# Optimization experiments

Measured on AMD Instinct MI355X. Metric: run time of the kernel, lower is better.

## Reference

```python
import jax, jax.numpy as jnp
import numpy as np
import math

NH = 16  # n_head
HS = 64  # head_size = n_embd // n_head


def setup_inputs() -> dict:
    key = jax.random.key(0)
    ks = jax.random.split(key, 7)
    B, T, C, QL, KVL = 2, 2048, 1024, 128, 128
    s = lambda k, shape, fan_in: jax.random.normal(k, shape, jnp.float32) / np.sqrt(fan_in)
    return {
        "x": jax.random.normal(ks[0], (B, T, C), jnp.float32),
        "W_dq": s(ks[1], (QL, C), C),
        "W_uq": s(ks[2], (C, QL), QL),
        "W_dkv": s(ks[3], (KVL, C), C),
        "W_uk": s(ks[4], (C, KVL), KVL),
        "W_uv": s(ks[5], (C, KVL), KVL),
        "W_o": s(ks[6], (C, C), C),
    }


def reference(x, W_dq, W_uq, W_dkv, W_uk, W_uv, W_o):
    B, T, C = x.shape
    kvl = W_dkv.shape[0]
    # absorbed matrices (training branch)
    k_eff = (W_dq.T @ W_uq.T @ W_uk).reshape(NH, HS, kvl)            # (nh, hs, kvl)
    v_eff = (W_uv.T @ W_o.T).reshape(kvl, NH, HS).transpose(1, 0, 2)  # (nh, kvl, hs)
    # latent kv cache
    c_kv = x @ W_dkv.T                                                # (B, T, kvl)
    # query path
    q = (x @ W_dq.T @ W_uq.T).reshape(B, T, NH, HS).transpose(0, 2, 1, 3)  # (B, nh, T, hs)
    # scores: q @ k_eff @ c_kv^T
    ql = jnp.einsum('bhtd,hdl->bhtl', q, k_eff)                       # (B, nh, T, kvl)
    scores = jnp.einsum('bhtl,bsl->bhts', ql, c_kv) / math.sqrt(HS)   # (B, nh, T, T)
    # causal mask
    mask = jnp.tril(jnp.ones((T, T), dtype=bool))
    scores = jnp.where(mask[None, None], scores, -jnp.inf)
    attn = jax.nn.softmax(scores, axis=-1)
    # output: attn @ c_kv @ v_eff
    ctx = jnp.einsum('bhts,bsl->bhtl', attn, c_kv)                    # (B, nh, T, kvl)
    y = jnp.einsum('bhtl,hld->bhtd', ctx, v_eff)                      # (B, nh, T, hs)
    y = y.transpose(0, 2, 1, 3).reshape(B, T, C)
    return y, c_kv
```

## Files before the change

### kernel.cpp

```cpp
#include <hip/hip_runtime.h>
#include <hip/hip_bf16.h>

typedef __hip_bfloat16 bf16;
typedef __attribute__((ext_vector_type(8))) short short8;
typedef __attribute__((ext_vector_type(4))) float f32x4;

#define NHD 16
#define HSD 64
#define KVLD 128
#define QLD 128
#define CD 1024
#define BD 2
#define TD 2048

__device__ __forceinline__ short8 ld8(const bf16* p) { return *(const short8*)p; }
__device__ __forceinline__ void st8(bf16* p, short8 v) { *(short8*)p = v; }

__device__ __forceinline__ void st4(bf16* p, float4 a) {
    union { short4 s; bf16 h[4]; } u;
    u.h[0] = __float2bfloat16(a.x); u.h[1] = __float2bfloat16(a.y);
    u.h[2] = __float2bfloat16(a.z); u.h[3] = __float2bfloat16(a.w);
    *(short4*)p = u.s;
}
__device__ __forceinline__ void st4f(bf16* p, f32x4 a) {
    union { short4 s; bf16 h[4]; } u;
    u.h[0] = __float2bfloat16(a[0]); u.h[1] = __float2bfloat16(a[1]);
    u.h[2] = __float2bfloat16(a[2]); u.h[3] = __float2bfloat16(a[3]);
    *(short4*)p = u.s;
}

__global__ __launch_bounds__(256) void k_pre(const float* __restrict__ wuq,
                                             const float* __restrict__ wuk,
                                             const float* __restrict__ wdq,
                                             const float* __restrict__ wdkv,
                                             float* __restrict__ m1p,
                                             float* __restrict__ G,
                                             bf16* __restrict__ wqkv_bf) {
    const int b = blockIdx.x;
    const int tid = threadIdx.x;
    if (b < 128) {
        const int part = b >> 4, ig = b & 15;
        const int i = ig * 8 + (tid >> 5);
        const int j4 = (tid & 31) << 2;
        const float* wq = wuq + (size_t)part * 128 * QLD;
        const float* wk = wuk + (size_t)part * 128 * KVLD;
        float4 acc = make_float4(0.f, 0.f, 0.f, 0.f);
        for (int c0 = 0; c0 < 128; c0 += 8) {
            float a[8]; float4 kv[8];
#pragma unroll
            for (int u = 0; u < 8; ++u) {
                a[u] = wq[(c0 + u) * QLD + i];
                kv[u] = *(const float4*)(wk + (c0 + u) * KVLD + j4);
            }
#pragma unroll
            for (int u = 0; u < 8; ++u) {
                acc.x = fmaf(a[u], kv[u].x, acc.x);
                acc.y = fmaf(a[u], kv[u].y, acc.y);
                acc.z = fmaf(a[u], kv[u].z, acc.z);
                acc.w = fmaf(a[u], kv[u].w, acc.w);
            }
        }
        *(float4*)(m1p + (size_t)part * 16384 + (size_t)i * 128 + j4) = acc;
    } else if (b < 256) {
        const int b1 = b - 128;
        const int h = b1 >> 3, p8 = b1 & 7;
        const int p = p8 * 16 + (tid >> 4);
        const int i8 = (tid & 15) << 3;
        float acc[8];
#pragma unroll
        for (int t = 0; t < 8; ++t) acc[t] = 0.f;
        const float* wdqp = wdq + (size_t)p * CD + h * 64;
        const float* wuqh = wuq + (size_t)(h * 64) * QLD + i8;
        for (int d0 = 0; d0 < 64; d0 += 8) {
            float a[8]; float4 b0[8], b1v[8];
#pragma unroll
            for (int u = 0; u < 8; ++u) {
                a[u] = wdqp[d0 + u];
                b0[u] = *(const float4*)(wuqh + (d0 + u) * QLD);
                b1v[u] = *(const float4*)(wuqh + (d0 + u) * QLD + 4);
            }
#pragma unroll
            for (int u = 0; u < 8; ++u) {
                acc[0] = fmaf(a[u], b0[u].x, acc[0]);  acc[1] = fmaf(a[u], b0[u].y, acc[1]);
                acc[2] = fmaf(a[u], b0[u].z, acc[2]);  acc[3] = fmaf(a[u], b0[u].w, acc[3]);
                acc[4] = fmaf(a[u], b1v[u].x, acc[4]); acc[5] = fmaf(a[u], b1v[u].y, acc[5]);
                acc[6] = fmaf(a[u], b1v[u].z, acc[6]); acc[7] = fmaf(a[u], b1v[u].w, acc[7]);
            }
        }
        float* dst = G + (size_t)h * 16384 + (size_t)p * 128 + i8;
        *(float4*)dst = make_float4(acc[0], acc[1], acc[2], acc[3]);
        *(float4*)(dst + 4) = make_float4(acc[4], acc[5], acc[6], acc[7]);
    } else {
        const int r = (b - 256) * 4 + (tid >> 6);
        const int lane = tid & 63;
        const float* src = (r < 128) ? (wdq + (size_t)r * CD) : (wdkv + (size_t)(r - 128) * CD);
        float4 f[4];
#pragma unroll
        for (int k = 0; k < 4; ++k) f[k] = ((const float4*)src)[lane + k * 64];
#pragma unroll
        for (int k = 0; k < 4; ++k)
            st4(wqkv_bf + (size_t)r * CD + (lane + k * 64) * 4, f[k]);
    }
}

__global__ __launch_bounds__(256) void k_main(const float* __restrict__ x,
                                              const bf16* __restrict__ wqkv_bf,
                                              const float* __restrict__ m1p,
                                              const float* __restrict__ G,
                                              const float* __restrict__ wuv,
                                              const float* __restrict__ wo,
                                              bf16* __restrict__ q1_bf,
                                              float* __restrict__ ckv_out,
                                              bf16* __restrict__ ckv_bf,
                                              bf16* __restrict__ ckvT_bf,
                                              bf16* __restrict__ Et_bf,
                                              bf16* __restrict__ veffT_bf) {
    __shared__ __align__(16) char arena[49152];
    const int blk = blockIdx.x;
    const int tid = threadIdx.x;

    if (blk < 256) {
        const int m0 = blk * 16;
        const int w = tid >> 6, lane = tid & 63, m16 = lane & 15, g = lane >> 4;
        bf16* As = (bf16*)arena;
        bf16* Bs = (bf16*)(arena + 2304);

        const int arow = tid >> 4, akc = (tid & 15) << 2;
        const float* axp = x + (size_t)(m0 + arow) * CD + akc;
        int brow[8], bkc[8];
#pragma unroll
        for (int kk = 0; kk < 8; ++kk) {
            int v = tid + kk * 256;
            brow[kk] = v >> 3; bkc[kk] = (v & 7) << 3;
        }

        float4 pA = *(const float4*)(axp);
        short8 pB[8];
#pragma unroll
        for (int kk = 0; kk < 8; ++kk)
            pB[kk] = ld8(wqkv_bf + (size_t)brow[kk] * CD + bkc[kk]);

        f32x4 acc[4];
#pragma unroll
        for (int nb = 0; nb < 4; ++nb) acc[nb] = (f32x4){0.f, 0.f, 0.f, 0.f};

        for (int k0 = 0; k0 < CD; k0 += 64) {
            __syncthreads();
            st4(As + arow * 72 + akc, pA);
#pragma unroll
            for (int kk = 0; kk < 8; ++kk)
                st8(Bs + brow[kk] * 72 + bkc[kk], pB[kk]);
            __syncthreads();
            if (k0 + 64 < CD) {
                pA = *(const float4*)(axp + k0 + 64);
#pragma unroll
                for (int kk = 0; kk < 8; ++kk)
                    pB[kk] = ld8(wqkv_bf + (size_t)brow[kk] * CD + k0 + 64 + bkc[kk]);
            }
            short8 aF[2];
#pragma unroll
            for (int kf = 0; kf < 2; ++kf)
                aF[kf] = ld8(As + m16 * 72 + kf * 32 + g * 8);
#pragma unroll
            for (int nb = 0; nb < 4; ++nb)
#pragma unroll
                for (int kf = 0; kf < 2; ++kf) {
                    short8 bF = ld8(Bs + (w * 64 + nb * 16 + m16) * 72 + kf * 32 + g * 8);
                    acc[nb] = __builtin_amdgcn_mfma_f32_16x16x32_bf16(aF[kf], bF, acc[nb], 0, 0, 0);
                }
        }

        const int bb = m0 >> 11;
        const int tl0 = (m0 & 2047) + g * 4;
#pragma unroll
        for (int nb = 0; nb < 4; ++nb) {
            int col = w * 64 + nb * 16 + m16;
            if (col < 128) {
#pragma unroll
                for (int r = 0; r < 4; ++r)
                    q1_bf[(size_t)(m0 + g * 4 + r) * QLD + col] = __float2bfloat16(acc[nb][r]);
            } else {
                int l = col - 128;
                union { short4 s; bf16 h[4]; } pk;
#pragma unroll
                for (int r = 0; r < 4; ++r) {
                    int t = m0 + g * 4 + r;
                    float v = acc[nb][r];
                    ckv_out[(size_t)t * KVLD + l] = v;
                    bf16 hv = __float2bfloat16(v);
                    ckv_bf[(size_t)t * KVLD + l] = hv;
                    pk.h[r] = hv;
                }
                *(short4*)(ckvT_bf + ((size_t)bb * KVLD + l) * TD + tl0) = pk.s;
            }
        }
    } else if (blk < 512) {
        const int b2 = blk - 256;
        const int h = b2 >> 4, lb = b2 & 15;
        float* m1s = (float*)arena;
        for (int v = tid; v < 1024; v += 256) {
            int p = v >> 3, lq = v & 7;
            float t0[8];
#pragma unroll
            for (int part = 0; part < 8; ++part)
                t0[part] = m1p[(size_t)part * 16384 + (size_t)p * 128 + lb * 8 + lq];
            float s0 = 0.f;
#pragma unroll
            for (int part = 0; part < 8; ++part) s0 += t0[part];
            m1s[v] = s0;
        }
        __syncthreads();
        const int lq = tid >> 5, i4 = (tid & 31) << 2;
        const float* Gh = G + (size_t)h * 16384;
        float4 acc = make_float4(0.f, 0.f, 0.f, 0.f);
        for (int p0 = 0; p0 < 128; p0 += 8) {
            float4 g[8]; float a[8];
#pragma unroll
            for (int u = 0; u < 8; ++u) {
                g[u] = *(const float4*)(Gh + (p0 + u) * 128 + i4);
                a[u] = m1s[(p0 + u) * 8 + lq];
            }
#pragma unroll
            for (int u = 0; u < 8; ++u) {
                acc.x = fmaf(a[u], g[u].x, acc.x);
                acc.y = fmaf(a[u], g[u].y, acc.y);
                acc.z = fmaf(a[u], g[u].z, acc.z);
                acc.w = fmaf(a[u], g[u].w, acc.w);
            }
        }
        const float sc = 0.1803368801f;
        const int l = lb * 8 + lq;
        st4(Et_bf + ((size_t)h * 128 + l) * 128 + i4,
            make_float4(sc * acc.x, sc * acc.y, sc * acc.z, sc * acc.w));
    } else {
        const int b3 = blk - 512;
        const int cc0 = b3 * 4;
        float* woS = (float*)arena;
        float* wuvS = (float*)arena + 4096;
#pragma unroll
        for (int k = 0; k < 4; ++k)
            ((float4*)woS)[tid + k * 256] = ((const float4*)(wo + (size_t)cc0 * CD))[tid + k * 256];

        const int r = tid >> 6;
        const int lh = tid & 63;
        float4 pf[8];
#pragma unroll
        for (int t = 0; t < 8; ++t)
            pf[t] = ((const float4*)wuv)[t * 256 + tid];

        float a0 = 0.f, a1 = 0.f;
        for (int ch = 0; ch < 16; ++ch) {
            __syncthreads();
#pragma unroll
            for (int t = 0; t < 8; ++t)
                ((float4*)wuvS)[t * 256 + tid] = pf[t];
            __syncthreads();
            if (ch < 15) {
#pragma unroll
                for (int t = 0; t < 8; ++t)
                    pf[t] = ((const float4*)wuv)[(ch + 1) * 2048 + t * 256 + tid];
            }
            const float* wr = woS + r * 1024 + ch * 64;
            const float2* vv = (const float2*)wuvS + lh;
            for (int cb = 0; cb < 64; cb += 8) {
                float wv[8]; float2 v[8];
#pragma unroll
                for (int u = 0; u < 8; ++u) {
                    wv[u] = wr[cb + u];
                    v[u] = vv[(cb + u) * 64];
                }
#pragma unroll
                for (int u = 0; u < 8; ++u) {
                    a0 = fmaf(wv[u], v[u].x, a0);
                    a1 = fmaf(wv[u], v[u].y, a1);
                }
            }
        }
        union { short2 s; bf16 h2[2]; } u;
        u.h2[0] = __float2bfloat16(a0);
        u.h2[1] = __float2bfloat16(a1);
        *(short2*)(veffT_bf + (size_t)(cc0 + r) * KVLD + lh * 2) = u.s;
    }
}

__global__ __launch_bounds__(512, 4) void k_flash(const bf16* __restrict__ Q1_bf,
                                                  const bf16* __restrict__ Et_bf,
                                                  const bf16* __restrict__ ckv_bf,
                                                  const bf16* __restrict__ ckvT_bf,
                                                  const bf16* __restrict__ veffT_bf,
                                                  float* __restrict__ yout) {
    const int h = blockIdx.x & 15;
    const int b = blockIdx.x >> 4;
    const int qlo = blockIdx.y;
    const int qhi = 31 - qlo;
    const int tid = threadIdx.x;
    const int w = tid >> 6;
    const int ws = w >> 2;
    const int wq = w & 3;
    const int lane = tid & 63;
    const int m16 = lane & 15;
    const int g = lane >> 4;
    const int myqt = ws ? qlo : qhi;
    const int row0 = myqt * 64;

    __shared__ __align__(16) short smem_raw[28288];
    bf16* smem = (bf16*)smem_raw;
    bf16* kvN = smem;
    bf16* kvT = smem + 8704;
    bf16* pS  = smem + 19072 + w * 1152;
    bf16* bufLo = kvT;
    bf16* vT = smem + 19072;

    {
        const bf16 one = __float2bfloat16(1.0f);
        for (int idx = tid; idx < 16 * 72; idx += 512)
            kvT[9216 + idx] = one;
    }

    {
        const bf16* q1hi = Q1_bf + ((size_t)(b * TD + qhi * 64)) * QLD;
        const bf16* q1lo = Q1_bf + ((size_t)(b * TD + qlo * 64)) * QLD;
#pragma unroll
        for (int k = 0; k < 2; ++k) {
            int v = tid + k * 512;
            int row = v >> 4, cv = (v & 15) << 3;
            st8(kvN + row * 136 + cv, ld8(q1hi + row * QLD + cv));
            st8(bufLo + row * 136 + cv, ld8(q1lo + row * QLD + cv));
        }
    }
    __syncthreads();
    bf16* myQ1 = ws ? bufLo : kvN;
    {
        short8 aq[4];
#pragma unroll
        for (int kf = 0; kf < 4; ++kf)
            aq[kf] = ld8(myQ1 + (wq * 16 + m16) * 136 + kf * 32 + g * 8);
        const bf16* Eh = Et_bf + (size_t)h * QLD * KVLD;
        f32x4 qc[8];
#pragma unroll
        for (int nb = 0; nb < 8; ++nb) qc[nb] = (f32x4){0.f, 0.f, 0.f, 0.f};
#pragma unroll
        for (int nb = 0; nb < 8; ++nb)
#pragma unroll
            for (int kf = 0; kf < 4; ++kf) {
                short8 bq = ld8(Eh + (nb * 16 + m16) * QLD + kf * 32 + g * 8);
                qc[nb] = __builtin_amdgcn_mfma_f32_16x16x32_bf16(bq, aq[kf], qc[nb], 0, 0, 0);
            }
        __syncthreads();
#pragma unroll
        for (int nb = 0; nb < 8; ++nb)
            st4f(myQ1 + (wq * 16 + m16) * 136 + nb * 16 + g * 4, qc[nb]);
    }
    __syncthreads();
    short8 qlA[4];
#pragma unroll
    for (int kf = 0; kf < 4; ++kf)
        qlA[kf] = ld8(myQ1 + (wq * 16 + m16) * 136 + kf * 32 + g * 8);

    f32x4 cx[9];
#pragma unroll
    for (int nb = 0; nb < 9; ++nb) cx[nb] = (f32x4){0.f, 0.f, 0.f, 0.f};
    float mrow = -INFINITY;
    const int rg = row0 + wq * 16 + m16;

    const bf16* ckb = ckv_bf + (size_t)b * TD * KVLD;
    const bf16* ckTb = ckvT_bf + (size_t)b * KVLD * TD;

    int nrow[2], ncol[2], trow[2], tcol[2];
#pragma unroll
    for (int k = 0; k < 2; ++k) {
        int v = tid + k * 512;
        nrow[k] = v >> 4; ncol[k] = (v & 15) << 3;
        trow[k] = v >> 3; tcol[k] = (v & 7) << 3;
    }
    short8 pfN[2], pfT[2];
#pragma unroll
    for (int k = 0; k < 2; ++k) {
        pfN[k] = ld8(ckb + (size_t)nrow[k] * KVLD + ncol[k]);
        pfT[k] = ld8(ckTb + (size_t)trow[k] * TD + tcol[k]);
    }

    for (int tile = 0; tile <= qhi; ++tile) {
        const int s0 = tile * 64;
        __syncthreads();
#pragma unroll
        for (int k = 0; k < 2; ++k) {
            st8(kvN + nrow[k] * 136 + ncol[k], pfN[k]);
            st8(kvT + trow[k] * 72 + tcol[k], pfT[k]);
        }
        __syncthreads();
        if (tile < qhi) {
            const int s1 = s0 + 64;
#pragma unroll
            for (int k = 0; k < 2; ++k) {
                pfN[k] = ld8(ckb + (size_t)(s1 + nrow[k]) * KVLD + ncol[k]);
                pfT[k] = ld8(ckTb + (size_t)trow[k] * TD + s1 + tcol[k]);
            }
        }

        if (ws == 0 || tile <= qlo) {
            f32x4 sa[4];
#pragma unroll
            for (int nb = 0; nb < 4; ++nb) sa[nb] = (f32x4){0.f, 0.f, 0.f, 0.f};
#pragma unroll
            for (int nb = 0; nb < 4; ++nb)
#pragma unroll
                for (int kf = 0; kf < 4; ++kf) {
                    short8 ak = ld8(kvN + (nb * 16 + m16) * 136 + kf * 32 + g * 8);
                    sa[nb] = __builtin_amdgcn_mfma_f32_16x16x32_bf16(ak, qlA[kf], sa[nb], 0, 0, 0);
                }

            if (tile == myqt) {
#pragma unroll
                for (int nb = 0; nb < 4; ++nb)
#pragma unroll
                    for (int r = 0; r < 4; ++r) {
                        int sg = s0 + nb * 16 + g * 4 + r;
                        if (sg > rg) sa[nb][r] = -INFINITY;
                    }
            }

            float mloc = sa[0][0];
#pragma unroll
            for (int nb = 0; nb < 4; ++nb)
#pragma unroll
                for (int r = 0; r < 4; ++r) mloc = fmaxf(mloc, sa[nb][r]);
            mloc = fmaxf(mloc, __shfl_xor(mloc, 16));
            mloc = fmaxf(mloc, __shfl_xor(mloc, 32));
            if (__any(mloc > mrow + 8.f)) {
                float mt = fmaxf(mrow, mloc);
                float al = exp2f(mrow - mt);
                mrow = mt;
#pragma unroll
                for (int nb = 0; nb < 9; ++nb)
#pragma unroll
                    for (int r = 0; r < 4; ++r) cx[nb][r] *= al;
            }

#pragma unroll
            for (int nb = 0; nb < 4; ++nb) {
                float4 p4;
                p4.x = exp2f(sa[nb][0] - mrow);
                p4.y = exp2f(sa[nb][1] - mrow);
                p4.z = exp2f(sa[nb][2] - mrow);
                p4.w = exp2f(sa[nb][3] - mrow);
                st4(pS + m16 * 72 + nb * 16 + g * 4, p4);
            }
            __builtin_amdgcn_wave_barrier();

            short8 pA[2];
#pragma unroll
            for (int kf = 0; kf < 2; ++kf)
                pA[kf] = ld8(pS + m16 * 72 + kf * 32 + g * 8);
#pragma unroll
            for (int nb = 0; nb < 9; ++nb)
#pragma unroll
                for (int kf = 0; kf < 2; ++kf) {
                    short8 av = ld8(kvT + (nb * 16 + m16) * 72 + kf * 32 + g * 8);
                    cx[nb] = __builtin_amdgcn_mfma_f32_16x16x32_bf16(av, pA[kf], cx[nb], 0, 0, 0);
                }
        }
    }

    float invl = 1.f / cx[8][0];
#pragma unroll
    for (int nb = 0; nb < 8; ++nb)
#pragma unroll
        for (int r = 0; r < 4; ++r) cx[nb][r] *= invl;
    __syncthreads();
    bf16* ctxS = ws ? bufLo : kvN;
#pragma unroll
    for (int nb = 0; nb < 8; ++nb)
        st4f(ctxS + (wq * 16 + m16) * 136 + nb * 16 + g * 4, cx[nb]);
    {
        const bf16* vsrc = veffT_bf + (size_t)h * HSD * KVLD;
#pragma unroll
        for (int k = 0; k < 2; ++k) {
            int v = tid + k * 512;
            int row = v >> 4, cv = (v & 15) << 3;
            st8(vT + row * 136 + cv, ld8(vsrc + row * KVLD + cv));
        }
    }
    __syncthreads();

    short8 cB[4];
#pragma unroll
    for (int kf = 0; kf < 4; ++kf)
        cB[kf] = ld8(ctxS + (wq * 16 + m16) * 136 + kf * 32 + g * 8);
    f32x4 ya[4];
#pragma unroll
    for (int nb = 0; nb < 4; ++nb) ya[nb] = (f32x4){0.f, 0.f, 0.f, 0.f};
#pragma unroll
    for (int nb = 0; nb < 4; ++nb)
#pragma unroll
        for (int kf = 0; kf < 4; ++kf) {
            short8 av = ld8(vT + (nb * 16 + m16) * 136 + kf * 32 + g * 8);
            ya[nb] = __builtin_amdgcn_mfma_f32_16x16x32_bf16(av, cB[kf], ya[nb], 0, 0, 0);
        }
    float* yo = yout + ((size_t)b * TD + rg) * CD + h * HSD;
#pragma unroll
    for (int nb = 0; nb < 4; ++nb)
        *(float4*)(yo + nb * 16 + g * 4) = *(float4*)&ya[nb];
}

extern "C" void kernel_launch(void* const* d_in, const int* in_sizes, int n_in,
                              void* d_out, int out_size, void* d_ws, size_t ws_size,
                              hipStream_t stream) {
    const float* x    = (const float*)d_in[0];
    const float* wdq  = (const float*)d_in[1];
    const float* wuq  = (const float*)d_in[2];
    const float* wdkv = (const float*)d_in[3];
    const float* wuk  = (const float*)d_in[4];
    const float* wuv  = (const float*)d_in[5];
    const float* wo   = (const float*)d_in[6];
    float* yout = (float*)d_out;
    float* ckv_out = yout + (size_t)BD * TD * CD;

    float* ws = (float*)d_ws;
    float* M1P = ws;
    float* G   = M1P + 131072;
    bf16* wqkv_bf  = (bf16*)(G + 262144);
    bf16* Et_bf    = wqkv_bf + 262144;
    bf16* veffT_bf = Et_bf + 262144;
    bf16* ckv_bf   = veffT_bf + 131072;
    bf16* ckvT_bf  = ckv_bf + 524288;
    bf16* Q1_bf    = ckvT_bf + 524288;

    k_pre <<<320, 256, 0, stream>>>(wuq, wuk, wdq, wdkv, M1P, G, wqkv_bf);
    k_main<<<768, 256, 0, stream>>>(x, wqkv_bf, M1P, G, wuv, wo,
                                    Q1_bf, ckv_out, ckv_bf, ckvT_bf, Et_bf, veffT_bf);

    dim3 grid(32, 16);
    k_flash<<<grid, 512, 0, stream>>>(Q1_bf, Et_bf, ckv_bf, ckvT_bf, veffT_bf, yout);
}
```

Before: 221.1 us.

## Compute softmax denominator in registers, move v_eff prep to k_pre, add MFMA priority

The flash kernel no longer gets the row sum from a ninth MFMA block against a ones row in shared memory. It now accumulates the denominator from the exponentials with two cross-lane shuffles, which removes one of nine PV MFMA groups per tile and shrinks shared memory. The v_eff transpose product moves from k_main into k_pre, so k_main uses less LDS and launches fewer blocks, while k_pre grows and its blocks need 48KB LDS. s_setprio wraps the MFMA loops to favour matrix issue across waves.

```diff
diff --git a/kernel.cpp b/kernel.cpp
--- a/kernel.cpp
+++ b/kernel.cpp
@@ -33,9 +33,13 @@
                                              const float* __restrict__ wuk,
                                              const float* __restrict__ wdq,
                                              const float* __restrict__ wdkv,
+                                             const float* __restrict__ wuv,
+                                             const float* __restrict__ wo,
                                              float* __restrict__ m1p,
                                              float* __restrict__ G,
-                                             bf16* __restrict__ wqkv_bf) {
+                                             bf16* __restrict__ wqkv_bf,
+                                             bf16* __restrict__ veffT_bf) {
+    __shared__ __align__(16) char arena[49152];
     const int b = blockIdx.x;
     const int tid = threadIdx.x;
     if (b < 128) {
@@ -90,7 +94,7 @@
         float* dst = G + (size_t)h * 16384 + (size_t)p * 128 + i8;
         *(float4*)dst = make_float4(acc[0], acc[1], acc[2], acc[3]);
         *(float4*)(dst + 4) = make_float4(acc[4], acc[5], acc[6], acc[7]);
-    } else {
+    } else if (b < 320) {
         const int r = (b - 256) * 4 + (tid >> 6);
         const int lane = tid & 63;
         const float* src = (r < 128) ? (wdq + (size_t)r * CD) : (wdkv + (size_t)(r - 128) * CD);
@@ -100,6 +104,54 @@
 #pragma unroll
         for (int k = 0; k < 4; ++k)
             st4(wqkv_bf + (size_t)r * CD + (lane + k * 64) * 4, f[k]);
+    } else {
+        const int b3 = b - 320;
+        const int cc0 = b3 * 4;
+        float* woS = (float*)arena;
+        float* wuvS = (float*)arena + 4096;
+#pragma unroll
+        for (int k = 0; k < 4; ++k)
+            ((float4*)woS)[tid + k * 256] = ((const float4*)(wo + (size_t)cc0 * CD))[tid + k * 256];
+
+        const int r = tid >> 6;
+        const int lh = tid & 63;
+        float4 pf[8];
+#pragma unroll
+        for (int t = 0; t < 8; ++t)
+            pf[t] = ((const float4*)wuv)[t * 256 + tid];
+
+        float a0 = 0.f, a1 = 0.f;
+        for (int ch = 0; ch < 16; ++ch) {
+            __syncthreads();
+#pragma unroll
+            for (int t = 0; t < 8; ++t)
+                ((float4*)wuvS)[t * 256 + tid] = pf[t];
+            __syncthreads();
+            if (ch < 15) {
+#pragma unroll
+                for (int t = 0; t < 8; ++t)
+                    pf[t] = ((const float4*)wuv)[(ch + 1) * 2048 + t * 256 + tid];
+            }
+            const float* wr = woS + r * 1024 + ch * 64;
+            const float2* vv = (const float2*)wuvS + lh;
+            for (int cb = 0; cb < 64; cb += 8) {
+                float wv[8]; float2 v[8];
+#pragma unroll
+                for (int u = 0; u < 8; ++u) {
+                    wv[u] = wr[cb + u];
+                    v[u] = vv[(cb + u) * 64];
+                }
+#pragma unroll
+                for (int u = 0; u < 8; ++u) {
+                    a0 = fmaf(wv[u], v[u].x, a0);
+                    a1 = fmaf(wv[u], v[u].y, a1);
+                }
+            }
+        }
+        union { short2 s; bf16 h2[2]; } u;
+        u.h2[0] = __float2bfloat16(a0);
+        u.h2[1] = __float2bfloat16(a1);
+        *(short2*)(veffT_bf + (size_t)(cc0 + r) * KVLD + lh * 2) = u.s;
     }
 }
 
@@ -107,15 +159,12 @@
                                               const bf16* __restrict__ wqkv_bf,
                                               const float* __restrict__ m1p,
                                               const float* __restrict__ G,
-                                              const float* __restrict__ wuv,
-                                              const float* __restrict__ wo,
                                               bf16* __restrict__ q1_bf,
                                               float* __restrict__ ckv_out,
                                               bf16* __restrict__ ckv_bf,
                                               bf16* __restrict__ ckvT_bf,
-                                              bf16* __restrict__ Et_bf,
-                                              bf16* __restrict__ veffT_bf) {
-    __shared__ __align__(16) char arena[49152];
+                                              bf16* __restrict__ Et_bf) {
+    __shared__ __align__(16) char arena[39168];
     const int blk = blockIdx.x;
     const int tid = threadIdx.x;
 
@@ -194,7 +243,7 @@
                 *(short4*)(ckvT_bf + ((size_t)bb * KVLD + l) * TD + tl0) = pk.s;
             }
         }
-    } else if (blk < 512) {
+    } else {
         const int b2 = blk - 256;
         const int h = b2 >> 4, lb = b2 & 15;
         float* m1s = (float*)arena;
@@ -232,54 +281,6 @@
         const int l = lb * 8 + lq;
         st4(Et_bf + ((size_t)h * 128 + l) * 128 + i4,
             make_float4(sc * acc.x, sc * acc.y, sc * acc.z, sc * acc.w));
-    } else {
-        const int b3 = blk - 512;
-        const int cc0 = b3 * 4;
-        float* woS = (float*)arena;
-        float* wuvS = (float*)arena + 4096;
-#pragma unroll
-        for (int k = 0; k < 4; ++k)
-            ((float4*)woS)[tid + k * 256] = ((const float4*)(wo + (size_t)cc0 * CD))[tid + k * 256];
-
-        const int r = tid >> 6;
-        const int lh = tid & 63;
-        float4 pf[8];
-#pragma unroll
-        for (int t = 0; t < 8; ++t)
-            pf[t] = ((const float4*)wuv)[t * 256 + tid];
-
-        float a0 = 0.f, a1 = 0.f;
-        for (int ch = 0; ch < 16; ++ch) {
-            __syncthreads();
-#pragma unroll
-            for (int t = 0; t < 8; ++t)
-                ((float4*)wuvS)[t * 256 + tid] = pf[t];
-            __syncthreads();
-            if (ch < 15) {
-#pragma unroll
-                for (int t = 0; t < 8; ++t)
-                    pf[t] = ((const float4*)wuv)[(ch + 1) * 2048 + t * 256 + tid];
-            }
-            const float* wr = woS + r * 1024 + ch * 64;
-            const float2* vv = (const float2*)wuvS + lh;
-            for (int cb = 0; cb < 64; cb += 8) {
-                float wv[8]; float2 v[8];
-#pragma unroll
-                for (int u = 0; u < 8; ++u) {
-                    wv[u] = wr[cb + u];
-                    v[u] = vv[(cb + u) * 64];
-                }
-#pragma unroll
-                for (int u = 0; u < 8; ++u) {
-                    a0 = fmaf(wv[u], v[u].x, a0);
-                    a1 = fmaf(wv[u], v[u].y, a1);
-                }
-            }
-        }
-        union { short2 s; bf16 h2[2]; } u;
-        u.h2[0] = __float2bfloat16(a0);
-        u.h2[1] = __float2bfloat16(a1);
-        *(short2*)(veffT_bf + (size_t)(cc0 + r) * KVLD + lh * 2) = u.s;
     }
 }
 
@@ -303,19 +304,13 @@
     const int myqt = ws ? qlo : qhi;
     const int row0 = myqt * 64;
 
-    __shared__ __align__(16) short smem_raw[28288];
+    __shared__ __align__(16) short smem_raw[27136];
     bf16* smem = (bf16*)smem_raw;
     bf16* kvN = smem;
     bf16* kvT = smem + 8704;
-    bf16* pS  = smem + 19072 + w * 1152;
+    bf16* pS  = smem + 17920 + w * 1152;
     bf16* bufLo = kvT;
-    bf16* vT = smem + 19072;
-
-    {
-        const bf16 one = __float2bfloat16(1.0f);
-        for (int idx = tid; idx < 16 * 72; idx += 512)
-            kvT[9216 + idx] = one;
-    }
+    bf16* vT = smem + 17920;
 
     {
         const bf16* q1hi = Q1_bf + ((size_t)(b * TD + qhi * 64)) * QLD;
@@ -357,9 +352,10 @@
     for (int kf = 0; kf < 4; ++kf)
         qlA[kf] = ld8(myQ1 + (wq * 16 + m16) * 136 + kf * 32 + g * 8);
 
-    f32x4 cx[9];
-#pragma unroll
-    for (int nb = 0; nb < 9; ++nb) cx[nb] = (f32x4){0.f, 0.f, 0.f, 0.f};
+    f32x4 cx[8];
+#pragma unroll
+    for (int nb = 0; nb < 8; ++nb) cx[nb] = (f32x4){0.f, 0.f, 0.f, 0.f};
+    float den = 0.f;
     float mrow = -INFINITY;
     const int rg = row0 + wq * 16 + m16;
 
@@ -402,6 +398,7 @@
             f32x4 sa[4];
 #pragma unroll
             for (int nb = 0; nb < 4; ++nb) sa[nb] = (f32x4){0.f, 0.f, 0.f, 0.f};
+            __builtin_amdgcn_s_setprio(1);
 #pragma unroll
             for (int nb = 0; nb < 4; ++nb)
 #pragma unroll
@@ -409,6 +406,7 @@
                     short8 ak = ld8(kvN + (nb * 16 + m16) * 136 + kf * 32 + g * 8);
                     sa[nb] = __builtin_amdgcn_mfma_f32_16x16x32_bf16(ak, qlA[kf], sa[nb], 0, 0, 0);
                 }
+            __builtin_amdgcn_s_setprio(0);
 
             if (tile == myqt) {
 #pragma unroll
@@ -431,12 +429,14 @@
                 float mt = fmaxf(mrow, mloc);
                 float al = exp2f(mrow - mt);
                 mrow = mt;
-#pragma unroll
-                for (int nb = 0; nb < 9; ++nb)
+                den *= al;
+#pragma unroll
+                for (int nb = 0; nb < 8; ++nb)
 #pragma unroll
                     for (int r = 0; r < 4; ++r) cx[nb][r] *= al;
             }
 
+            float psum = 0.f;
 #pragma unroll
             for (int nb = 0; nb < 4; ++nb) {
                 float4 p4;
@@ -444,25 +444,31 @@
                 p4.y = exp2f(sa[nb][1] - mrow);
                 p4.z = exp2f(sa[nb][2] - mrow);
                 p4.w = exp2f(sa[nb][3] - mrow);
+                psum += (p4.x + p4.y) + (p4.z + p4.w);
                 st4(pS + m16 * 72 + nb * 16 + g * 4, p4);
             }
+            psum += __shfl_xor(psum, 16);
+            psum += __shfl_xor(psum, 32);
+            den += psum;
             __builtin_amdgcn_wave_barrier();
 
             short8 pA[2];
 #pragma unroll
             for (int kf = 0; kf < 2; ++kf)
                 pA[kf] = ld8(pS + m16 * 72 + kf * 32 + g * 8);
-#pragma unroll
-            for (int nb = 0; nb < 9; ++nb)
+            __builtin_amdgcn_s_setprio(1);
+#pragma unroll
+            for (int nb = 0; nb < 8; ++nb)
 #pragma unroll
                 for (int kf = 0; kf < 2; ++kf) {
                     short8 av = ld8(kvT + (nb * 16 + m16) * 72 + kf * 32 + g * 8);
                     cx[nb] = __builtin_amdgcn_mfma_f32_16x16x32_bf16(av, pA[kf], cx[nb], 0, 0, 0);
                 }
-        }
-    }
-
-    float invl = 1.f / cx[8][0];
+            __builtin_amdgcn_s_setprio(0);
+        }
+    }
+
+    float invl = 1.f / den;
 #pragma unroll
     for (int nb = 0; nb < 8; ++nb)
 #pragma unroll
@@ -526,9 +532,10 @@
     bf16* ckvT_bf  = ckv_bf + 524288;
     bf16* Q1_bf    = ckvT_bf + 524288;
 
-    k_pre <<<320, 256, 0, stream>>>(wuq, wuk, wdq, wdkv, M1P, G, wqkv_bf);
-    k_main<<<768, 256, 0, stream>>>(x, wqkv_bf, M1P, G, wuv, wo,
-                                    Q1_bf, ckv_out, ckv_bf, ckvT_bf, Et_bf, veffT_bf);
+    k_pre <<<576, 256, 0, stream>>>(wuq, wuk, wdq, wdkv, wuv, wo,
+                                    M1P, G, wqkv_bf, veffT_bf);
+    k_main<<<512, 256, 0, stream>>>(x, wqkv_bf, M1P, G,
+                                    Q1_bf, ckv_out, ckv_bf, ckvT_bf, Et_bf);
 
     dim3 grid(32, 16);
     k_flash<<<grid, 512, 0, stream>>>(Q1_bf, Et_bf, ckv_bf, ckvT_bf, veffT_bf, yout);
```

Result: no change. 224.7 us (+1.6%).

## Split paired causal tiles into per-tile blocks and shuffle P through registers

Applied to the files above, without the earlier changes.

Each flash block now handles a single 64-row query tile with 256 threads, instead of pairing a high and a low tile in a 512-thread block. The grid doubles and is ordered heaviest-first. The softmax denominator is now summed explicitly in registers, replacing the extra all-ones column MFMA (9 to 8 output blocks). P is moved between lanes with cross-lane shuffles into MFMA operand layout instead of going through a per-wave LDS scratch buffer. This removes LDS round-trips and an MFMA per tile and cuts shared memory per block, at the cost of losing the balanced pairing and adding many shuffle instructions.

```diff
diff --git a/kernel.cpp b/kernel.cpp
--- a/kernel.cpp
+++ b/kernel.cpp
@@ -27,6 +27,11 @@
     u.h[0] = __float2bfloat16(a[0]); u.h[1] = __float2bfloat16(a[1]);
     u.h[2] = __float2bfloat16(a[2]); u.h[3] = __float2bfloat16(a[3]);
     *(short4*)p = u.s;
+}
+__device__ __forceinline__ unsigned pk2(float x, float y) {
+    union { unsigned u; bf16 h[2]; } t;
+    t.h[0] = __float2bfloat16(x); t.h[1] = __float2bfloat16(y);
+    return t.u;
 }
 
 __global__ __launch_bounds__(256) void k_pre(const float* __restrict__ wuq,
@@ -283,7 +288,7 @@
     }
 }
 
-__global__ __launch_bounds__(512, 4) void k_flash(const bf16* __restrict__ Q1_bf,
+__global__ __launch_bounds__(256, 4) void k_flash(const bf16* __restrict__ Q1_bf,
                                                   const bf16* __restrict__ Et_bf,
                                                   const bf16* __restrict__ ckv_bf,
                                                   const bf16* __restrict__ ckvT_bf,
@@ -291,50 +296,35 @@
                                                   float* __restrict__ yout) {
     const int h = blockIdx.x & 15;
     const int b = blockIdx.x >> 4;
-    const int qlo = blockIdx.y;
-    const int qhi = 31 - qlo;
+    const int qt = 31 - blockIdx.y;
     const int tid = threadIdx.x;
-    const int w = tid >> 6;
-    const int ws = w >> 2;
-    const int wq = w & 3;
+    const int wq = tid >> 6;
     const int lane = tid & 63;
     const int m16 = lane & 15;
     const int g = lane >> 4;
-    const int myqt = ws ? qlo : qhi;
-    const int row0 = myqt * 64;
-
-    __shared__ __align__(16) short smem_raw[28288];
+    const int row0 = qt * 64;
+
+    __shared__ __align__(16) short smem_raw[17920];
     bf16* smem = (bf16*)smem_raw;
     bf16* kvN = smem;
     bf16* kvT = smem + 8704;
-    bf16* pS  = smem + 19072 + w * 1152;
-    bf16* bufLo = kvT;
-    bf16* vT = smem + 19072;
+    bf16* vT  = kvT;
 
     {
-        const bf16 one = __float2bfloat16(1.0f);
-        for (int idx = tid; idx < 16 * 72; idx += 512)
-            kvT[9216 + idx] = one;
-    }
-
-    {
-        const bf16* q1hi = Q1_bf + ((size_t)(b * TD + qhi * 64)) * QLD;
-        const bf16* q1lo = Q1_bf + ((size_t)(b * TD + qlo * 64)) * QLD;
-#pragma unroll
-        for (int k = 0; k < 2; ++k) {
-            int v = tid + k * 512;
+        const bf16* q1p = Q1_bf + ((size_t)(b * TD + row0)) * QLD;
+#pragma unroll
+        for (int k = 0; k < 4; ++k) {
+            int v = tid + k * 256;
             int row = v >> 4, cv = (v & 15) << 3;
-            st8(kvN + row * 136 + cv, ld8(q1hi + row * QLD + cv));
-            st8(bufLo + row * 136 + cv, ld8(q1lo + row * QLD + cv));
+            st8(kvN + row * 136 + cv, ld8(q1p + row * QLD + cv));
         }
     }
     __syncthreads();
-    bf16* myQ1 = ws ? bufLo : kvN;
     {
         short8 aq[4];
 #pragma unroll
         for (int kf = 0; kf < 4; ++kf)
-            aq[kf] = ld8(myQ1 + (wq * 16 + m16) * 136 + kf * 32 + g * 8);
+            aq[kf] = ld8(kvN + (wq * 16 + m16) * 136 + kf * 32 + g * 8);
         const bf16* Eh = Et_bf + (size_t)h * QLD * KVLD;
         f32x4 qc[8];
 #pragma unroll
@@ -349,134 +339,157 @@
         __syncthreads();
 #pragma unroll
         for (int nb = 0; nb < 8; ++nb)
-            st4f(myQ1 + (wq * 16 + m16) * 136 + nb * 16 + g * 4, qc[nb]);
+            st4f(kvN + (wq * 16 + m16) * 136 + nb * 16 + g * 4, qc[nb]);
     }
     __syncthreads();
     short8 qlA[4];
 #pragma unroll
     for (int kf = 0; kf < 4; ++kf)
-        qlA[kf] = ld8(myQ1 + (wq * 16 + m16) * 136 + kf * 32 + g * 8);
-
-    f32x4 cx[9];
-#pragma unroll
-    for (int nb = 0; nb < 9; ++nb) cx[nb] = (f32x4){0.f, 0.f, 0.f, 0.f};
+        qlA[kf] = ld8(kvN + (wq * 16 + m16) * 136 + kf * 32 + g * 8);
+
+    f32x4 cx[8];
+#pragma unroll
+    for (int nb = 0; nb < 8; ++nb) cx[nb] = (f32x4){0.f, 0.f, 0.f, 0.f};
+    float den = 0.f;
     float mrow = -INFINITY;
     const int rg = row0 + wq * 16 + m16;
 
     const bf16* ckb = ckv_bf + (size_t)b * TD * KVLD;
     const bf16* ckTb = ckvT_bf + (size_t)b * KVLD * TD;
 
-    int nrow[2], ncol[2], trow[2], tcol[2];
-#pragma unroll
-    for (int k = 0; k < 2; ++k) {
-        int v = tid + k * 512;
+    int nrow[4], ncol[4], trow[4], tcol[4];
+#pragma unroll
+    for (int k = 0; k < 4; ++k) {
+        int v = tid + k * 256;
         nrow[k] = v >> 4; ncol[k] = (v & 15) << 3;
         trow[k] = v >> 3; tcol[k] = (v & 7) << 3;
     }
-    short8 pfN[2], pfT[2];
-#pragma unroll
-    for (int k = 0; k < 2; ++k) {
+    short8 pfN[4], pfT[4];
+#pragma unroll
+    for (int k = 0; k < 4; ++k) {
         pfN[k] = ld8(ckb + (size_t)nrow[k] * KVLD + ncol[k]);
         pfT[k] = ld8(ckTb + (size_t)trow[k] * TD + tcol[k]);
     }
 
-    for (int tile = 0; tile <= qhi; ++tile) {
-        const int s0 = tile * 64;
+    const int sA = (((2 * g) & 3) << 4) + m16;
+    const int sB = (((2 * g + 1) & 3) << 4) + m16;
+    const int hi = g >> 1;
+
+    for (int tile = 0; tile <= qt; ++tile) {
         __syncthreads();
 #pragma unroll
-        for (int k = 0; k < 2; ++k) {
+        for (int k = 0; k < 4; ++k) {
             st8(kvN + nrow[k] * 136 + ncol[k], pfN[k]);
             st8(kvT + trow[k] * 72 + tcol[k], pfT[k]);
         }
         __syncthreads();
-        if (tile < qhi) {
-            const int s1 = s0 + 64;
-#pragma unroll
-            for (int k = 0; k < 2; ++k) {
+        if (tile < qt) {
+            const int s1 = (tile + 1) * 64;
+#pragma unroll
+            for (int k = 0; k < 4; ++k) {
                 pfN[k] = ld8(ckb + (size_t)(s1 + nrow[k]) * KVLD + ncol[k]);
                 pfT[k] = ld8(ckTb + (size_t)trow[k] * TD + s1 + tcol[k]);
             }
         }
 
-        if (ws == 0 || tile <= qlo) {
-            f32x4 sa[4];
-#pragma unroll
-            for (int nb = 0; nb < 4; ++nb) sa[nb] = (f32x4){0.f, 0.f, 0.f, 0.f};
+        f32x4 sa[4];
+#pragma unroll
+        for (int nb = 0; nb < 4; ++nb) sa[nb] = (f32x4){0.f, 0.f, 0.f, 0.f};
+#pragma unroll
+        for (int nb = 0; nb < 4; ++nb)
+#pragma unroll
+            for (int kf = 0; kf < 4; ++kf) {
+                short8 ak = ld8(kvN + (nb * 16 + m16) * 136 + kf * 32 + g * 8);
+                sa[nb] = __builtin_amdgcn_mfma_f32_16x16x32_bf16(ak, qlA[kf], sa[nb], 0, 0, 0);
+            }
+
+        if (tile == qt) {
+            const int s0 = tile * 64;
 #pragma unroll
             for (int nb = 0; nb < 4; ++nb)
 #pragma unroll
-                for (int kf = 0; kf < 4; ++kf) {
-                    short8 ak = ld8(kvN + (nb * 16 + m16) * 136 + kf * 32 + g * 8);
-                    sa[nb] = __builtin_amdgcn_mfma_f32_16x16x32_bf16(ak, qlA[kf], sa[nb], 0, 0, 0);
+                for (int r = 0; r < 4; ++r) {
+                    int sg = s0 + nb * 16 + g * 4 + r;
+                    if (sg > rg) sa[nb][r] = -INFINITY;
                 }
-
-            if (tile == myqt) {
-#pragma unroll
-                for (int nb = 0; nb < 4; ++nb)
-#pragma unroll
-                    for (int r = 0; r < 4; ++r) {
-                        int sg = s0 + nb * 16 + g * 4 + r;
-                        if (sg > rg) sa[nb][r] = -INFINITY;
-                    }
-            }
-
-            float mloc = sa[0][0];
-#pragma unroll
-            for (int nb = 0; nb < 4; ++nb)
-#pragma unroll
-                for (int r = 0; r < 4; ++r) mloc = fmaxf(mloc, sa[nb][r]);
-            mloc = fmaxf(mloc, __shfl_xor(mloc, 16));
-            mloc = fmaxf(mloc, __shfl_xor(mloc, 32));
-            if (__any(mloc > mrow + 8.f)) {
-                float mt = fmaxf(mrow, mloc);
-                float al = exp2f(mrow - mt);
-                mrow = mt;
-#pragma unroll
-                for (int nb = 0; nb < 9; ++nb)
-#pragma unroll
-                    for (int r = 0; r < 4; ++r) cx[nb][r] *= al;
-            }
-
-#pragma unroll
-            for (int nb = 0; nb < 4; ++nb) {
-                float4 p4;
-                p4.x = exp2f(sa[nb][0] - mrow);
-                p4.y = exp2f(sa[nb][1] - mrow);
-                p4.z = exp2f(sa[nb][2] - mrow);
-                p4.w = exp2f(sa[nb][3] - mrow);
-                st4(pS + m16 * 72 + nb * 16 + g * 4, p4);
-            }
-            __builtin_amdgcn_wave_barrier();
-
-            short8 pA[2];
-#pragma unroll
-            for (int kf = 0; kf < 2; ++kf)
-                pA[kf] = ld8(pS + m16 * 72 + kf * 32 + g * 8);
-#pragma unroll
-            for (int nb = 0; nb < 9; ++nb)
-#pragma unroll
-                for (int kf = 0; kf < 2; ++kf) {
-                    short8 av = ld8(kvT + (nb * 16 + m16) * 72 + kf * 32 + g * 8);
-                    cx[nb] = __builtin_amdgcn_mfma_f32_16x16x32_bf16(av, pA[kf], cx[nb], 0, 0, 0);
-                }
-        }
-    }
-
-    float invl = 1.f / cx[8][0];
+        }
+
+        float mloc = sa[0][0];
+#pragma unroll
+        for (int nb = 0; nb < 4; ++nb)
+#pragma unroll
+            for (int r = 0; r < 4; ++r) mloc = fmaxf(mloc, sa[nb][r]);
+        mloc = fmaxf(mloc, __shfl_xor(mloc, 16));
+        mloc = fmaxf(mloc, __shfl_xor(mloc, 32));
+        if (__any(mloc > mrow + 8.f)) {
+            float mt = fmaxf(mrow, mloc);
+            float al = exp2f(mrow - mt);
+            mrow = mt;
+            den *= al;
+#pragma unroll
+            for (int nb = 0; nb < 8; ++nb)
+#pragma unroll
+                for (int r = 0; r < 4; ++r) cx[nb][r] *= al;
+        }
+
+        unsigned w_[4][2];
+        float psum = 0.f;
+#pragma unroll
+        for (int nb = 0; nb < 4; ++nb) {
+            float p0 = exp2f(sa[nb][0] - mrow);
+            float p1 = exp2f(sa[nb][1] - mrow);
+            float p2 = exp2f(sa[nb][2] - mrow);
+            float p3 = exp2f(sa[nb][3] - mrow);
+            psum += (p0 + p1) + (p2 + p3);
+            w_[nb][0] = pk2(p0, p1);
+            w_[nb][1] = pk2(p2, p3);
+        }
+        psum += __shfl_xor(psum, 16);
+        psum += __shfl_xor(psum, 32);
+        den += psum;
+
+        short8 pA[2];
+#pragma unroll
+        for (int kf = 0; kf < 2; ++kf) {
+            unsigned a0 = (unsigned)__shfl((int)w_[2 * kf][0], sA);
+            unsigned b0 = (unsigned)__shfl((int)w_[2 * kf + 1][0], sA);
+            unsigned a1 = (unsigned)__shfl((int)w_[2 * kf][1], sA);
+            unsigned b1 = (unsigned)__shfl((int)w_[2 * kf + 1][1], sA);
+            unsigned a2 = (unsigned)__shfl((int)w_[2 * kf][0], sB);
+            unsigned b2 = (unsigned)__shfl((int)w_[2 * kf + 1][0], sB);
+            unsigned a3 = (unsigned)__shfl((int)w_[2 * kf][1], sB);
+            unsigned b3 = (unsigned)__shfl((int)w_[2 * kf + 1][1], sB);
+            union { short8 s8; unsigned u[4]; } pb;
+            pb.u[0] = hi ? b0 : a0;
+            pb.u[1] = hi ? b1 : a1;
+            pb.u[2] = hi ? b2 : a2;
+            pb.u[3] = hi ? b3 : a3;
+            pA[kf] = pb.s8;
+        }
+
+#pragma unroll
+        for (int nb = 0; nb < 8; ++nb)
+#pragma unroll
+            for (int kf = 0; kf < 2; ++kf) {
+                short8 av = ld8(kvT + (nb * 16 + m16) * 72 + kf * 32 + g * 8);
+                cx[nb] = __builtin_amdgcn_mfma_f32_16x16x32_bf16(av, pA[kf], cx[nb], 0, 0, 0);
+            }
+    }
+
+    float invl = 1.f / den;
 #pragma unroll
     for (int nb = 0; nb < 8; ++nb)
 #pragma unroll
         for (int r = 0; r < 4; ++r) cx[nb][r] *= invl;
     __syncthreads();
-    bf16* ctxS = ws ? bufLo : kvN;
 #pragma unroll
     for (int nb = 0; nb < 8; ++nb)
-        st4f(ctxS + (wq * 16 + m16) * 136 + nb * 16 + g * 4, cx[nb]);
+        st4f(kvN + (wq * 16 + m16) * 136 + nb * 16 + g * 4, cx[nb]);
     {
         const bf16* vsrc = veffT_bf + (size_t)h * HSD * KVLD;
 #pragma unroll
-        for (int k = 0; k < 2; ++k) {
-            int v = tid + k * 512;
+        for (int k = 0; k < 4; ++k) {
+            int v = tid + k * 256;
             int row = v >> 4, cv = (v & 15) << 3;
             st8(vT + row * 136 + cv, ld8(vsrc + row * KVLD + cv));
         }
@@ -486,7 +499,7 @@
     short8 cB[4];
 #pragma unroll
     for (int kf = 0; kf < 4; ++kf)
-        cB[kf] = ld8(ctxS + (wq * 16 + m16) * 136 + kf * 32 + g * 8);
+        cB[kf] = ld8(kvN + (wq * 16 + m16) * 136 + kf * 32 + g * 8);
     f32x4 ya[4];
 #pragma unroll
     for (int nb = 0; nb < 4; ++nb) ya[nb] = (f32x4){0.f, 0.f, 0.f, 0.f};
@@ -530,6 +543,6 @@
     k_main<<<768, 256, 0, stream>>>(x, wqkv_bf, M1P, G, wuv, wo,
                                     Q1_bf, ckv_out, ckv_bf, ckvT_bf, Et_bf, veffT_bf);
 
-    dim3 grid(32, 16);
-    k_flash<<<grid, 512, 0, stream>>>(Q1_bf, Et_bf, ckv_bf, ckvT_bf, veffT_bf, yout);
-}
+    dim3 grid(32, 32);
+    k_flash<<<grid, 256, 0, stream>>>(Q1_bf, Et_bf, ckv_bf, ckvT_bf, veffT_bf, yout);
+}
```

Measured after the change: 288.0 us. +30.2%, slower.
